# Kernel tuning notes

Hardware: AMD Instinct MI355X
Metric: run time of the kernel (lower is better)

## Reference

```python
import jax, jax.numpy as jnp
import numpy as np

# dims: batch, history P, horizon Q, hidden D, nodes N, cells C=H*W, Z channels
B_, P_, Q_, D_, N_, C_, H_, W_, CZ = 16, 12, 12, 64, 2000, 1024, 32, 32, 2
K_DIFF = 3  # max diffusion step of DCGRUCell -> K+1 Chebyshev terms


def _mlp2(x, w1, b1, w2, b2):
    return jax.nn.relu(x @ w1 + b1) @ w2 + b2


def _st_embedding(SE, TE, sw1, sb1, sw2, sb2, tw1, tb1, tw2, tb2):
    # GMAN-style spatio-temporal embedding: SE (M,D), TE (B,P,2) ints
    se = _mlp2(SE, sw1, sb1, sw2, sb2)                                  # (M, D)
    te = jnp.concatenate([jax.nn.one_hot(TE[..., 0], 7, dtype=SE.dtype),
                          jax.nn.one_hot(TE[..., 1], 288, dtype=SE.dtype)], axis=-1)
    te = _mlp2(te, tw1, tb1, tw2, tb2)                                  # (B, P, D)
    return se[None, None] + te[:, :, None, :]                           # (B, P, M, D)


def _scaled_laplacian(adj):
    # DCRNN 'laplacian' filter: L_tilde = 2 L / lambda_max - I, lambda_max ~= 2
    A = jnp.maximum(adj, adj.T)
    d = A.sum(axis=1)
    dinv = jnp.where(d > 0, jax.lax.rsqrt(d), 0.0)
    eye = jnp.eye(A.shape[0], dtype=A.dtype)
    L = eye - (dinv[:, None] * A) * dinv[None, :]
    return L - eye


def _gconv(x, L, K):
    # Chebyshev diffusion features: x (B,N,F) -> (B,N,F*(K+1))
    xs = [x, jnp.einsum('nm,bmf->bnf', L, x)]
    for _ in range(2, K + 1):
        xs.append(2.0 * jnp.einsum('nm,bmf->bnf', L, xs[-1]) - xs[-2])
    b, n, f = x.shape
    return jnp.stack(xs, axis=-1).reshape(b, n, f * (K + 1))


def _hard_sigmoid(x):
    return jnp.clip(0.2 * x + 0.5, 0.0, 1.0)


def _conv2d(x, w):
    return jax.lax.conv_general_dilated(x, w, (1, 1), 'SAME',
        dimension_numbers=('NHWC', 'HWIO', 'NHWC'))


def _forward(X, Z, TE, adj_gg, adj_gr, gumbel_noise, se_x, se_z, movement_logits,
             stex_se_w1, stex_se_b1, stex_se_w2, stex_se_b2,
             stex_te_w1, stex_te_b1, stex_te_w2, stex_te_b2,
             stez_se_w1, stez_se_b1, stez_se_w2, stez_se_b2,
             stez_te_w1, stez_te_b1, stez_te_w2, stez_te_b2,
             fcs_z_w1, fcs_z_b1, fcs_z_w2, fcs_z_b2,
             fcs_x_in_w1, fcs_x_in_b1, fcs_x_in_w2, fcs_x_in_b2,
             mov_fc_w, mov_fc_b,
             fcs_x_out_w1, fcs_x_out_b1, fcs_x_out_w2, fcs_x_out_b2,
             convlstm_wx, convlstm_wh,
             dcgru_gate_w, dcgru_gate_b, dcgru_cand_w, dcgru_cand_b):
    B = X.shape[0]
    TEp = TE.astype(jnp.int32)[:, :P_, :]
    # --- cell branch ---
    STEZ = _st_embedding(se_z, TEp, stez_se_w1, stez_se_b1, stez_se_w2, stez_se_b2,
                         stez_te_w1, stez_te_b1, stez_te_w2, stez_te_b2)
    Zf = _mlp2(Z, fcs_z_w1, fcs_z_b1, fcs_z_w2, fcs_z_b2) + STEZ          # (B,P,C,D)
    Zg = Zf.reshape(B, P_, H_, W_, D_)
    def clstm_step(carry, x):
        h, c = carry
        gates = _conv2d(x, convlstm_wx) + _conv2d(h, convlstm_wh)         # (B,H,W,4D)
        i, f, g, o = jnp.split(gates, 4, axis=-1)
        c = _hard_sigmoid(f) * c + _hard_sigmoid(i) * jnp.tanh(g)
        h = _hard_sigmoid(o) * jnp.tanh(c)
        return (h, c), h
    hc0 = (jnp.zeros((B, H_, W_, D_), X.dtype), jnp.zeros((B, H_, W_, D_), X.dtype))
    _, hs = jax.lax.scan(clstm_step, hc0, jnp.swapaxes(Zg, 0, 1))
    Zc = jnp.swapaxes(hs, 0, 1).reshape(B, P_, C_, D_)
    # gumbel-softmax routing over cells (soft, tau=1)
    g = -jnp.log(-jnp.log(gumbel_noise + 1e-20) + 1e-20)
    mZ = jax.nn.softmax(movement_logits + g, axis=-1)                     # (C,C)
    Zc = jnp.einsum('cd,bpdk->bpck', mZ, Zc)
    Zc = jax.nn.relu(Zc @ mov_fc_w + mov_fc_b)
    ZX = jnp.einsum('nc,bpck->bpnk', adj_gr, Zc)                          # (B,P,N,D)
    # --- node branch ---
    STEX = _st_embedding(se_x, TEp, stex_se_w1, stex_se_b1, stex_se_w2, stex_se_b2,
                         stex_te_w1, stex_te_b1, stex_te_w2, stex_te_b2)
    Xf = _mlp2(X[..., None], fcs_x_in_w1, fcs_x_in_b1, fcs_x_in_w2, fcs_x_in_b2) + STEX + ZX
    L = _scaled_laplacian(adj_gg)
    def dcgru_step(h, x):
        xh = jnp.concatenate([x, h], axis=-1)                             # (B,N,2D)
        ru = jax.nn.sigmoid(_gconv(xh, L, K_DIFF) @ dcgru_gate_w + dcgru_gate_b)
        r, u = jnp.split(ru, 2, axis=-1)
        cnd = jnp.tanh(_gconv(jnp.concatenate([x, r * h], axis=-1), L, K_DIFF)
                       @ dcgru_cand_w + dcgru_cand_b)
        return u * h + (1.0 - u) * cnd, None
    h_last, _ = jax.lax.scan(dcgru_step, jnp.zeros((B, N_, D_), X.dtype),
                             jnp.swapaxes(Xf, 0, 1))                      # (B,N,D)
    Y = _mlp2(h_last, fcs_x_out_w1, fcs_x_out_b1, fcs_x_out_w2, fcs_x_out_b2)  # (B,N,Q)
    return jnp.transpose(Y, (0, 2, 1))                                    # (B,Q,N)


def setup_inputs() -> dict:
    key = jax.random.key(0)
    ks = iter(jax.random.split(key, 64))
    def rn(shape, s=0.05):
        return jax.random.normal(next(ks), shape, dtype=jnp.float32) * s
    def ru(shape):
        return jax.random.uniform(next(ks), shape, dtype=jnp.float32)
    z = lambda *s: jnp.zeros(s, jnp.float32)
    NM = K_DIFF + 1
    inp = {
        'X': rn((B_, P_, N_), 1.0),
        'Z': rn((B_, P_, C_, CZ), 1.0),
        'TE': jax.random.randint(next(ks), (B_, P_ + Q_, 2), 0, 7, dtype=jnp.int32),
        'adj_gg': ru((N_, N_)),
        'adj_gr': ru((N_, C_)) * 0.01,
        'gumbel_noise': jnp.clip(ru((C_, C_)), 1e-6, 1.0 - 1e-6),
        'se_x': rn((N_, D_)), 'se_z': rn((C_, D_)),
        'movement_logits': rn((C_, C_)),
        'stex_se_w1': rn((D_, D_)), 'stex_se_b1': z(D_), 'stex_se_w2': rn((D_, D_)), 'stex_se_b2': z(D_),
        'stex_te_w1': rn((295, D_)), 'stex_te_b1': z(D_), 'stex_te_w2': rn((D_, D_)), 'stex_te_b2': z(D_),
        'stez_se_w1': rn((D_, D_)), 'stez_se_b1': z(D_), 'stez_se_w2': rn((D_, D_)), 'stez_se_b2': z(D_),
        'stez_te_w1': rn((295, D_)), 'stez_te_b1': z(D_), 'stez_te_w2': rn((D_, D_)), 'stez_te_b2': z(D_),
        'fcs_z_w1': rn((CZ, D_)), 'fcs_z_b1': z(D_), 'fcs_z_w2': rn((D_, D_)), 'fcs_z_b2': z(D_),
        'fcs_x_in_w1': rn((1, D_)), 'fcs_x_in_b1': z(D_), 'fcs_x_in_w2': rn((D_, D_)), 'fcs_x_in_b2': z(D_),
        'mov_fc_w': rn((D_, D_)), 'mov_fc_b': z(D_),
        'fcs_x_out_w1': rn((D_, D_)), 'fcs_x_out_b1': z(D_), 'fcs_x_out_w2': rn((D_, Q_)), 'fcs_x_out_b2': z(Q_),
        'convlstm_wx': rn((3, 3, D_, 4 * D_)), 'convlstm_wh': rn((3, 3, D_, 4 * D_)),
        'dcgru_gate_w': rn((2 * D_ * NM, 2 * D_)), 'dcgru_gate_b': z(2 * D_),
        'dcgru_cand_w': rn((2 * D_ * NM, D_)), 'dcgru_cand_b': z(D_),
    }
    return inp


def reference(X, Z, TE, adj_gg, adj_gr, gumbel_noise, se_x, se_z, movement_logits,
              stex_se_w1, stex_se_b1, stex_se_w2, stex_se_b2,
              stex_te_w1, stex_te_b1, stex_te_w2, stex_te_b2,
              stez_se_w1, stez_se_b1, stez_se_w2, stez_se_b2,
              stez_te_w1, stez_te_b1, stez_te_w2, stez_te_b2,
              fcs_z_w1, fcs_z_b1, fcs_z_w2, fcs_z_b2,
              fcs_x_in_w1, fcs_x_in_b1, fcs_x_in_w2, fcs_x_in_b2,
              mov_fc_w, mov_fc_b,
              fcs_x_out_w1, fcs_x_out_b1, fcs_x_out_w2, fcs_x_out_b2,
              convlstm_wx, convlstm_wh,
              dcgru_gate_w, dcgru_gate_b, dcgru_cand_w, dcgru_cand_b):
    return _forward(X, Z, TE, adj_gg, adj_gr, gumbel_noise, se_x, se_z, movement_logits,
                    stex_se_w1, stex_se_b1, stex_se_w2, stex_se_b2,
                    stex_te_w1, stex_te_b1, stex_te_w2, stex_te_b2,
                    stez_se_w1, stez_se_b1, stez_se_w2, stez_se_b2,
                    stez_te_w1, stez_te_b1, stez_te_w2, stez_te_b2,
                    fcs_z_w1, fcs_z_b1, fcs_z_w2, fcs_z_b2,
                    fcs_x_in_w1, fcs_x_in_b1, fcs_x_in_w2, fcs_x_in_b2,
                    mov_fc_w, mov_fc_b,
                    fcs_x_out_w1, fcs_x_out_b1, fcs_x_out_w2, fcs_x_out_b2,
                    convlstm_wx, convlstm_wh,
                    dcgru_gate_w, dcgru_gate_b, dcgru_cand_w, dcgru_cand_b)
```

## Files before the change

kernel.cpp:

```cpp
#include <hip/hip_runtime.h>
#include <hip/hip_bf16.h>
#include <math.h>

typedef _Float16 fp16;
typedef _Float16 f16x8 __attribute__((ext_vector_type(8)));
typedef float f32x4 __attribute__((ext_vector_type(4)));

#define BB 16
#define PP 12
#define QQ 12
#define NN 2000
#define CC 1024
#define GP 34
#define GP2 1156

static __device__ __forceinline__ float ldf(float v) { return v; }
static __device__ __forceinline__ float ldf(fp16 v) { return (float)v; }
static __device__ __forceinline__ void stf(float* p, float v) { *p = v; }
static __device__ __forceinline__ void stf(fp16* p, float v) { *p = (fp16)v; }

static __device__ __forceinline__ void gload_lds16(const fp16* g, fp16* l) {
  __builtin_amdgcn_global_load_lds(
      (const __attribute__((address_space(1))) void*)g,
      (__attribute__((address_space(3))) void*)l, 16, 0, 0);
// ... 130 lines not shown
}

__global__ void k_add_stez(fp16* __restrict__ dst, const fp16* __restrict__ src,
                           const float* __restrict__ seZ, const float* __restrict__ teZ) {
  long long i = (long long)blockIdx.x * 256 + threadIdx.x;
  if (i >= (long long)BB * PP * CC * 64) return;
  int j = (int)(i & 63);
  long long row = i >> 6;
  int c = (int)(row & 1023);
  int bp = (int)(row >> 10);
  int pc = ((c >> 5) + 1) * GP + (c & 31) + 1;
  dst[((long long)bp * GP2 + pc) * 64 + j] =
      (fp16)((float)src[i] + seZ[c * 64 + j] + teZ[bp * 64 + j]);
}

template <typename TA, typename TB, typename TC>
__global__ __launch_bounds__(256) void gemm_t(
    const TA* __restrict__ A, int lda, long long sA,
    const TB* __restrict__ Bm, int ldb, long long sB,
    TC* Cm, int ldc, long long sC,
    const TC* S, long long sS,
    const float* __restrict__ bias,
    int M, int Ncols, int K, float alpha, float beta, int act) {
  int bz = blockIdx.z;
  A += (long long)bz * sA;
  Bm += (long long)bz * sB;
  Cm += (long long)bz * sC;
  if (S) S += (long long)bz * sS;
  const int row0 = blockIdx.x * 64, col0 = blockIdx.y * 64;
  __shared__ float As[16][68];
  __shared__ float Bs[16][68];
  int tid = threadIdx.x, tx = tid & 15, ty = tid >> 4;
  float acc[4][4] = {};
  for (int k0 = 0; k0 < K; k0 += 16) {
#pragma unroll
    for (int j = 0; j < 4; ++j) {
      int e = tid + 256 * j;
      int m = e >> 4, kk = e & 15;
      int gm = row0 + m;
      As[kk][m] = (gm < M) ? ldf(A[(long long)gm * lda + k0 + kk]) : 0.f;
    }
#pragma unroll
    for (int j = 0; j < 4; ++j) {
      int e = tid + 256 * j;
      int kk = e >> 6, n = e & 63;
      int gn = col0 + n;
      Bs[kk][n] = (gn < Ncols) ? ldf(Bm[(long long)(k0 + kk) * ldb + gn]) : 0.f;
    }
    __syncthreads();
#pragma unroll
    for (int kk = 0; kk < 16; ++kk) {
      float a[4], bb[4];
#pragma unroll
      for (int i = 0; i < 4; ++i) a[i] = As[kk][ty * 4 + i];
#pragma unroll
      for (int j = 0; j < 4; ++j) bb[j] = Bs[kk][tx * 4 + j];
#pragma unroll
      for (int i = 0; i < 4; ++i)
#pragma unroll
        for (int j = 0; j < 4; ++j) acc[i][j] = fmaf(a[i], bb[j], acc[i][j]);
    }
    __syncthreads();
  }
#pragma unroll
  for (int i = 0; i < 4; ++i) {
    int r = row0 + ty * 4 + i;
    if (r >= M) continue;
#pragma unroll
    for (int j = 0; j < 4; ++j) {
      int cn = col0 + tx * 4 + j;
      if (cn >= Ncols) continue;
      float v = alpha * acc[i][j];
      if (bias) v += bias[cn];
      if (S) v += beta * ldf(S[(long long)r * ldc + cn]);
      if (act == 1) v = fmaxf(v, 0.f);
      else if (act == 2) v = 1.f / (1.f + expf(-v));
      else if (act == 3) v = tanhf(v);
      stf(&Cm[(long long)r * ldc + cn], v);
    }
  }
}

template <int MT, int MODE>
__global__ __launch_bounds__(256) void mfma2(
    const fp16* __restrict__ A, int lda,
    const fp16* __restrict__ B, int ldb, long long bBatch, int bShift, long long bSlab,
    int bHi,
    fp16* __restrict__ C, int ldc, long long cBatch,
    const float* __restrict__ bias,
    fp16* __restrict__ rhOut, const fp16* __restrict__ hIn, long long xStride,
    const fp16* __restrict__ uIn, long long uStride,
    const fp16* __restrict__ xB, long long xZ,
    int M, int Ncols, int K, float alpha) {
  __shared__ fp16 As[MT][40];
  __shared__ fp16 Bs[64][40];
  const int z = blockIdx.z;
  const int gm0 = blockIdx.x * MT, n0 = blockIdx.y * 64;
  B += (long long)z * bBatch;
  C += (long long)z * cBatch;
  if (rhOut) rhOut += (long long)z * xStride;
  if (hIn) hIn += (long long)z * xStride;
  if (uIn) uIn += (long long)z * uStride;
  if (xB) xB += (long long)z * xZ;
  const int tid = threadIdx.x;
  const int lane = tid & 63, wv = tid >> 6;
  const int wr = wv >> 1, wc = wv & 1;
  const int quad = lane >> 4, ln = lane & 15;
  const unsigned bMask = (1u << bShift) - 1u;
  constexpr int WM = MT / 32;
  f32x4 acc[WM][2];
#pragma unroll
  for (int i = 0; i < WM; ++i)
#pragma unroll
    for (int j = 0; j < 2; ++j) acc[i][j] = (f32x4){0.f, 0.f, 0.f, 0.f};

  for (int k0 = 0; k0 < K; k0 += 32) {
#pragma unroll
    for (int i = 0; i < MT / 64; ++i) {
      int c = tid + 256 * i;
      int row = c >> 2, seg = c & 3;
      int gm = gm0 + row;
      int kk0 = k0 + seg * 8;
      const fp16* src = A + (long long)gm * lda + kk0;
      if (gm < M && kk0 + 8 <= K) {
        *(f16x8*)&As[row][seg * 8] = *(const f16x8*)src;
      } else {
#pragma unroll
        for (int j = 0; j < 8; ++j)
          As[row][seg * 8 + j] = (gm < M && kk0 + j < K) ? src[j] : (fp16)0.f;
      }
    }
    {
      int kk = k0 + (tid & 31);
      int ngrp = tid >> 5;
      int slab = (int)((unsigned)kk >> bShift);
      int kin = (int)((unsigned)kk & bMask);
      int col = kin + (kin >= 64 ? bHi : 0);
      int n = n0 + ngrp * 8;
      const fp16* src;
      if (xB && slab == 0 && kin < 64)
        src = xB + (long long)kin * 2048 + n;
      else
        src = B + (long long)slab * bSlab + (long long)col * ldb + n;
      if (kk < K && n + 8 <= Ncols) {
        f16x8 v = *(const f16x8*)src;
#pragma unroll
        for (int j = 0; j < 8; ++j) Bs[ngrp * 8 + j][tid & 31] = v[j];
      } else {
#pragma unroll
        for (int j = 0; j < 8; ++j)
          Bs[ngrp * 8 + j][tid & 31] = (kk < K && n + j < Ncols) ? src[j] : (fp16)0.f;
      }
    }
    __syncthreads();
    f16x8 af[WM], bf[2];
#pragma unroll
    for (int wm = 0; wm < WM; ++wm)
      af[wm] = *(const f16x8*)&As[wr * (MT / 2) + wm * 16 + ln][quad * 8];
#pragma unroll
    for (int wn = 0; wn < 2; ++wn)
      bf[wn] = *(const f16x8*)&Bs[wc * 32 + wn * 16 + ln][quad * 8];
#pragma unroll
    for (int wm = 0; wm < WM; ++wm)
#pragma unroll
      for (int wn = 0; wn < 2; ++wn)
        acc[wm][wn] =
            __builtin_amdgcn_mfma_f32_16x16x32_f16(af[wm], bf[wn], acc[wm][wn], 0, 0, 0);
    __syncthreads();
  }
#pragma unroll
  for (int wm = 0; wm < WM; ++wm) {
#pragma unroll
    for (int wn = 0; wn < 2; ++wn) {
#pragma unroll
      for (int r = 0; r < 4; ++r) {
        int gm = gm0 + wr * (MT / 2) + wm * 16 + quad * 4 + r;
        int gn = n0 + wc * 32 + wn * 16 + ln;
        if (gm < M && gn < Ncols) {
          float v = alpha * acc[wm][wn][r];
          v += bias[gm];
          if (MODE == 1) {
            v = 1.f / (1.f + expf(-v));
            C[(long long)gm * ldc + gn] = (fp16)v;
            if (gm < 64) {
              float h = (float)hIn[(long long)gm * 2048 + gn];
              rhOut[(long long)gm * 2048 + gn] = (fp16)(v * h);
            }
          } else {
            v = tanhf(v);
            float u = (float)uIn[(long long)(64 + gm) * NN + gn];
            long long ci = (long long)gm * ldc + gn;
            float h = (float)C[ci];
            C[ci] = (fp16)(u * h + (1.f - u) * v);
          }
        }
      }
    }
  }
}

template <int MT, int NT>
__global__ __launch_bounds__(256) void mfma3(
    const fp16* __restrict__ A, int lda, long long zA, int aMsh, long long aMslab,
    const fp16* __restrict__ B, int ldb, long long zB,
    fp16* __restrict__ C, int ldc, long long zC, int cMsh, long long cMslab, int cNsh,
    long long cNslab,
    const fp16* __restrict__ S, long long zS, float beta,
    const float* __restrict__ rowBias, long long zRB,
    const float* __restrict__ s2T, int s2ld,
    int M, int Ncols, int K, float alpha, int act) {
  __shared__ fp16 As[MT][40];
  __shared__ fp16 Bs[NT][40];
  const int z = blockIdx.z;
  const int gm0 = blockIdx.x * MT, n0 = blockIdx.y * NT;
  A += (long long)z * zA;
  B += (long long)z * zB;
  C += (long long)z * zC;
  if (S) S += (long long)z * zS;
  const int tid = threadIdx.x;
  const int lane = tid & 63, wv = tid >> 6;
  const int wr = wv >> 1, wc = wv & 1;
  const int quad = lane >> 4, ln = lane & 15;
  const unsigned aMmask = (1u << aMsh) - 1u;
  const unsigned cMmask = (1u << cMsh) - 1u;
  const unsigned cNmask = (1u << cNsh) - 1u;
  constexpr int WM = MT / 32, WN = NT / 32;
  f32x4 acc[WM][WN];
#pragma unroll
  for (int i = 0; i < WM; ++i)
#pragma unroll
    for (int j = 0; j < WN; ++j) acc[i][j] = (f32x4){0.f, 0.f, 0.f, 0.f};

  for (int k0 = 0; k0 < K; k0 += 32) {
#pragma unroll
    for (int i = 0; i < MT / 64; ++i) {
      int c = tid + 256 * i;
      int row = c >> 2, seg = c & 3;
      int gm = gm0 + row;
      int kk0 = k0 + seg * 8;
      const fp16* src = A + ((long long)((unsigned)gm >> aMsh)) * aMslab +
                        (long long)(gm & aMmask) * lda + kk0;
      if (gm < M && kk0 + 8 <= K) {
        *(f16x8*)&As[row][seg * 8] = *(const f16x8*)src;
      } else {
#pragma unroll
        for (int j = 0; j < 8; ++j)
          As[row][seg * 8 + j] = (gm < M && kk0 + j < K) ? src[j] : (fp16)0.f;
      }
    }
#pragma unroll
    for (int i = 0; i < NT / 64; ++i) {
      int c = tid + 256 * i;
      int n = c >> 2, seg = c & 3;
      int gn = n0 + n;
      int kk0 = k0 + seg * 8;
      const fp16* src = B + (long long)gn * ldb + kk0;
      if (gn < Ncols && kk0 + 8 <= K) {
        *(f16x8*)&Bs[n][seg * 8] = *(const f16x8*)src;
      } else {
#pragma unroll
        for (int j = 0; j < 8; ++j)
          Bs[n][seg * 8 + j] = (gn < Ncols && kk0 + j < K) ? src[j] : (fp16)0.f;
// ... 68 lines not shown
  const fp16* bSrc[NT / 64];
#pragma unroll
  for (int i = 0; i < MT / 64; ++i) {
    int c = i * 256 + tid;
    int row = c >> 2;
    int lseg = (c & 3) ^ (row & 3);
    int gm = gm0 + row;
    unsigned b = (unsigned)gm >> rsh;
    unsigned wi = (unsigned)gm & ((1u << rsh) - 1u);
    unsigned sel = wi >> ssh;
    unsigned r = wi & ((1u << ssh) - 1u);
    const fp16* ab = sel ? (base1 + (long long)b * z1) : (base0 + (long long)b * z0);
    aSrc[i] = ab + (long long)r * lda + lseg * 8;
  }
#pragma unroll
  for (int i = 0; i < NT / 64; ++i) {
    int c = i * 256 + tid;
    int row = c >> 2;
    int lseg = (c & 3) ^ (row & 3);
    bSrc[i] = B + (long long)(n0 + row) * ldb + lseg * 8;
  }

  f32x4 acc[WM][WN];
#pragma unroll
  for (int i = 0; i < WM; ++i)
#pragma unroll
    for (int j = 0; j < WN; ++j) acc[i][j] = (f32x4){0.f, 0.f, 0.f, 0.f};

  const int sw = (quad ^ (ln & 3)) << 3;

#pragma unroll
  for (int i = 0; i < MT / 64; ++i) gload_lds16(aSrc[i], &As[0][(i * 256 + tid) * 8]);
#pragma unroll
  for (int i = 0; i < NT / 64; ++i) gload_lds16(bSrc[i], &Bs[0][(i * 256 + tid) * 8]);

  const int nk = K >> 5;
  for (int t = 0; t < nk; ++t) {
    const int buf = t & 1;
    __syncthreads();
    if (t + 1 < nk) {
      const int k1 = (t + 1) * 32;
#pragma unroll
      for (int i = 0; i < MT / 64; ++i)
        gload_lds16(aSrc[i] + k1, &As[buf ^ 1][(i * 256 + tid) * 8]);
#pragma unroll
      for (int i = 0; i < NT / 64; ++i)
        gload_lds16(bSrc[i] + k1, &Bs[buf ^ 1][(i * 256 + tid) * 8]);
    }
    f16x8 af[WM], bf[WN];
#pragma unroll
    for (int wm = 0; wm < WM; ++wm) {
      int row = wr * (MT / 2) + wm * 16 + ln;
      af[wm] = *(const f16x8*)&As[buf][row * 32 + sw];
    }
#pragma unroll
    for (int wn = 0; wn < WN; ++wn) {
      int row = wc * (NT / 2) + wn * 16 + ln;
      bf[wn] = *(const f16x8*)&Bs[buf][row * 32 + sw];
    }
#pragma unroll
    for (int wm = 0; wm < WM; ++wm)
#pragma unroll
      for (int wn = 0; wn < WN; ++wn)
        acc[wm][wn] =
            __builtin_amdgcn_mfma_f32_16x16x32_f16(af[wm], bf[wn], acc[wm][wn], 0, 0, 0);
  }
#pragma unroll
  for (int wm = 0; wm < WM; ++wm)
#pragma unroll
    for (int wn = 0; wn < WN; ++wn)
#pragma unroll
      for (int r = 0; r < 4; ++r) {
        int gm = gm0 + wr * (MT / 2) + wm * 16 + quad * 4 + r;
        int gn = n0 + wc * (NT / 2) + wn * 16 + ln;
        long long ci = ((long long)((unsigned)gm >> cMsh)) * cMslab +
                       (long long)(gm & cMmask) * ldc +
                       ((long long)((unsigned)gn >> cNsh)) * cNslab + (gn & cNmask);
        float v = alpha * acc[wm][wn][r];
        if (S) v += beta * (float)S[ci];
        C[ci] = (fp16)v;
      }
}

__global__ __launch_bounds__(256) void k_zxt4(
    const fp16* __restrict__ A1, const fp16* __restrict__ B1,
    const fp16* __restrict__ A2, const fp16* __restrict__ B2,
    fp16* __restrict__ C, const float* __restrict__ teXb, const float* __restrict__ seX) {
  __shared__ fp16 As[2][64 * 32];
  __shared__ fp16 Bs[2][128 * 32];
  const int z = blockIdx.z;
  const int n0 = blockIdx.y * 128;
  A1 += (long long)z * 64 * 1024;
  B2 += (long long)z * 2048 * 64;
  C += (long long)z * 64 * 2048;
  teXb += z * 64;
  const int tid = threadIdx.x;
  const int lane = tid & 63, wv = tid >> 6;
  const int wr = wv >> 1, wc = wv & 1;
  const int quad = lane >> 4, ln = lane & 15;

  const fp16 *a1p, *a2p;
  {
    int row = tid >> 2;
    int lseg = (tid & 3) ^ (row & 3);
    a1p = A1 + (long long)row * 1024 + lseg * 8;
    a2p = A2 + (long long)row * 64 + lseg * 8;
  }
  const fp16 *b1p[2], *b2p[2];
#pragma unroll
  for (int i = 0; i < 2; ++i) {
    int c = tid + 256 * i;
    int row = c >> 2;
    int lseg = (c & 3) ^ (row & 3);
    b1p[i] = B1 + (long long)(n0 + row) * 1024 + lseg * 8;
    b2p[i] = B2 + (long long)(n0 + row) * 64 + lseg * 8;
  }
  f32x4 acc[2][4];
#pragma unroll
  for (int i = 0; i < 2; ++i)
#pragma unroll
    for (int j = 0; j < 4; ++j) acc[i][j] = (f32x4){0.f, 0.f, 0.f, 0.f};

  auto stage = [&](int t, int buf) {
    if (t < 32) {
      int k1 = t * 32;
      gload_lds16(a1p + k1, &As[buf][tid * 8]);
#pragma unroll
      for (int i = 0; i < 2; ++i)
        gload_lds16(b1p[i] + k1, &Bs[buf][(i * 256 + tid) * 8]);
    } else {
      int k1 = (t - 32) * 32;
      gload_lds16(a2p + k1, &As[buf][tid * 8]);
#pragma unroll
      for (int i = 0; i < 2; ++i)
        gload_lds16(b2p[i] + k1, &Bs[buf][(i * 256 + tid) * 8]);
    }
  };
  stage(0, 0);
  const int sw = (quad ^ (ln & 3)) << 3;
  for (int t = 0; t < 34; ++t) {
    const int buf = t & 1;
    __syncthreads();
    if (t + 1 < 34) stage(t + 1, buf ^ 1);
    f16x8 af[2], bf[4];
#pragma unroll
    for (int wm = 0; wm < 2; ++wm) {
      int row = wr * 32 + wm * 16 + ln;
      af[wm] = *(const f16x8*)&As[buf][row * 32 + sw];
    }
#pragma unroll
    for (int wn = 0; wn < 4; ++wn) {
      int row = wc * 64 + wn * 16 + ln;
      bf[wn] = *(const f16x8*)&Bs[buf][row * 32 + sw];
    }
#pragma unroll
    for (int wm = 0; wm < 2; ++wm)
#pragma unroll
      for (int wn = 0; wn < 4; ++wn)
        acc[wm][wn] =
            __builtin_amdgcn_mfma_f32_16x16x32_f16(af[wm], bf[wn], acc[wm][wn], 0, 0, 0);
  }
#pragma unroll
  for (int wm = 0; wm < 2; ++wm)
#pragma unroll
    for (int wn = 0; wn < 4; ++wn)
#pragma unroll
      for (int r = 0; r < 4; ++r) {
        int gm = wr * 32 + wm * 16 + quad * 4 + r;
        int gn = n0 + wc * 64 + wn * 16 + ln;
        float v = (gn < NN) ? (acc[wm][wn][r] + teXb[gm] + seX[(long long)gn * 64 + gm])
                            : 0.f;
        C[(long long)gm * 2048 + gn] = (fp16)v;
      }
}

__global__ __launch_bounds__(256) void k_conv4(
    const fp16* __restrict__ Zfp, const fp16* __restrict__ hp,
    const fp16* __restrict__ wcatT, fp16* __restrict__ gates, int p) {
  __shared__ fp16 As[2][128 * 32];
  __shared__ fp16 Bs[2][64 * 32];
  const int gm0 = blockIdx.x * 128, n0 = blockIdx.y * 64;
  const int tid = threadIdx.x;
  const int lane = tid & 63, wv = tid >> 6;
  const int wr = wv >> 1, wc = wv & 1;
  const int quad = lane >> 4, ln = lane & 15;

  long long aZ[2], aH[2];
#pragma unroll
  for (int i = 0; i < 2; ++i) {
    int c = tid + 256 * i;
    int row = c >> 2;
    int lseg = (c & 3) ^ (row & 3);
    int m = gm0 + row;
    int b = m >> 10, y = (m >> 5) & 31, x = m & 31;
    int pc = (y + 1) * GP + (x + 1);
    aZ[i] = ((long long)(b * PP + p) * GP2 + pc) * 64 + lseg * 8;
    aH[i] = ((long long)b * GP2 + pc) * 64 + lseg * 8;
  }
  const fp16* bBase;
  {
    int row = tid >> 2;
    int lseg = (tid & 3) ^ (row & 3);
    bBase = wcatT + (long long)(n0 + row) * 1152 + lseg * 8;
  }
  f32x4 acc[4][2];
#pragma unroll
  for (int i = 0; i < 4; ++i)
#pragma unroll
    for (int j = 0; j < 2; ++j) acc[i][j] = (f32x4){0.f, 0.f, 0.f, 0.f};

  auto stage = [&](int t, int buf) {
    int tap = (t >> 1) % 9, half = t & 1;
    int srcsel = t >= 18;
    int off = ((tap / 3 - 1) * GP + (tap % 3 - 1)) * 64 + half * 32;
#pragma unroll
    for (int i = 0; i < 2; ++i) {
      const fp16* src = srcsel ? (hp + aH[i] + off) : (Zfp + aZ[i] + off);
      gload_lds16(src, &As[buf][(i * 256 + tid) * 8]);
    }
    gload_lds16(bBase + t * 32, &Bs[buf][tid * 8]);
  };
  stage(0, 0);
  const int sw = (quad ^ (ln & 3)) << 3;
  for (int t = 0; t < 36; ++t) {
    const int buf = t & 1;
    __syncthreads();
    if (t + 1 < 36) stage(t + 1, buf ^ 1);
    f16x8 af[4], bf[2];
#pragma unroll
    for (int wm = 0; wm < 4; ++wm) {
      int row = wr * 64 + wm * 16 + ln;
      af[wm] = *(const f16x8*)&As[buf][row * 32 + sw];
    }
#pragma unroll
    for (int wn = 0; wn < 2; ++wn) {
      int row = wc * 32 + wn * 16 + ln;
      bf[wn] = *(const f16x8*)&Bs[buf][row * 32 + sw];
    }
#pragma unroll
    for (int wm = 0; wm < 4; ++wm)
#pragma unroll
      for (int wn = 0; wn < 2; ++wn)
        acc[wm][wn] =
            __builtin_amdgcn_mfma_f32_16x16x32_f16(af[wm], bf[wn], acc[wm][wn], 0, 0, 0);
  }
#pragma unroll
  for (int wm = 0; wm < 4; ++wm)
#pragma unroll
    for (int wn = 0; wn < 2; ++wn)
#pragma unroll
      for (int r = 0; r < 4; ++r) {
        int gm = gm0 + wr * 64 + wm * 16 + quad * 4 + r;
        int gn = n0 + wc * 32 + wn * 16 + ln;
        gates[(long long)gm * 256 + gn] = (fp16)acc[wm][wn][r];
      }
// ... 23 lines not shown

__global__ void k_tmat(const float* __restrict__ X, const float* __restrict__ w1,
                       const float* __restrict__ b1, fp16* __restrict__ T, long long nrows) {
  long long i = (long long)blockIdx.x * 256 + threadIdx.x;
  if (i >= nrows * 64) return;
  int j = (int)(i & 63);
  long long row = i >> 6;
  int z = (int)(row / NN);
  int n = (int)(row - (long long)z * NN);
  T[(((long long)z * 2048) + n) * 64 + j] = (fp16)fmaxf(X[row] * w1[j] + b1[j], 0.f);
}

__global__ void k_trT(const fp16* __restrict__ U0, float* __restrict__ htmp) {
  long long i = (long long)blockIdx.x * 256 + threadIdx.x;
  if (i >= (long long)BB * NN * 64) return;
  int d = (int)(i & 63);
  long long bn = i >> 6;
  int b = (int)(bn / NN);
  int n = (int)(bn % NN);
  htmp[i] = (float)U0[((long long)b * 192 + 64 + d) * 2048 + n];
}

__global__ void k_out(const float* __restrict__ Y, float* __restrict__ out) {
  int i = blockIdx.x * 256 + threadIdx.x;
  if (i >= BB * QQ * NN) return;
  int n = i % NN;
  int bq = i / NN;
  int b = bq / QQ, q = bq % QQ;
  out[i] = Y[((long long)b * NN + n) * 12 + q];
}

template <typename TA, typename TB, typename TC>
static void launch_gemm(hipStream_t stream, const TA* A, int lda, long long sA,
                        const TB* Bm, int ldb, long long sB, TC* Cm, int ldc, long long sC,
                        const TC* S, long long sS, const float* bias, int M, int Nc, int K,
                        float alpha, float beta, int act, int batch) {
  dim3 g((M + 63) / 64, (Nc + 63) / 64, batch);
  gemm_t<TA, TB, TC><<<g, dim3(256), 0, stream>>>(A, lda, sA, Bm, ldb, sB, Cm, ldc, sC, S,
                                                  sS, bias, M, Nc, K, alpha, beta, act);
}

extern "C" void kernel_launch(void* const* d_in, const int* in_sizes, int n_in,
                              void* d_out, int out_size, void* d_ws, size_t ws_size,
                              hipStream_t stream) {
  char* base = (char*)d_ws;
  size_t off = 0;
  auto alloc_bytes = [&](size_t nb) -> char* {
    char* p = base + off;
    off += (nb + 255) & ~(size_t)255;
    return p;
  };
  auto allocf = [&](size_t n) -> float* { return (float*)alloc_bytes(n * 4); };
  auto alloch = [&](size_t n) -> fp16* { return (fp16*)alloc_bytes(n * 2); };

  const float* X = (const float*)d_in[0];
  const float* Z = (const float*)d_in[1];
  const int* TE = (const int*)d_in[2];
  const float* adj_gg = (const float*)d_in[3];
  const float* adj_gr = (const float*)d_in[4];
  const float* gumbel = (const float*)d_in[5];
  const float* se_x = (const float*)d_in[6];
  const float* se_z = (const float*)d_in[7];
  const float* movement = (const float*)d_in[8];
  auto W = [&](int i) { return (const float*)d_in[i]; };

  fp16* wcatT = alloch((size_t)256 * 1152);
  fp16* gwT = alloch(128 * 512);
  fp16* cwT = alloch(64 * 512);
  fp16* w2T = alloch(64 * 64);
  fp16* w2mT = alloch(64 * 64);
  float* dinv = allocf(NN);
  fp16* LMall = alloch((size_t)6144 * 2048);
  fp16* mZh = alloch((size_t)CC * CC);
  fp16* agh2 = alloch((size_t)2048 * CC);
  float* seZ = allocf(CC * 64);
  float* teZ = allocf(BB * PP * 64);
  float* seX = allocf(NN * 64);
  float* teXb = allocf(BB * PP * 64);
  float* mtmp = allocf(NN * 64);
  float* tetmp = allocf(BB * PP * 64);
  fp16* ruT = alloch((size_t)BB * 128 * NN);
  char* pool = alloc_bytes(50331648);
  fp16* Uall = (fp16*)pool;
  fp16* Zftmp = (fp16*)pool;
  fp16* gates = (fp16*)pool;
  fp16* chh = (fp16*)(pool + 8388608);
  float* ccc = (float*)(pool + 12582912);
  fp16* Zmix = (fp16*)pool;
  fp16* ZmovT = (fp16*)(pool + 25165824);
  fp16* zpool = alloch((size_t)BB * PP * 64 * 2048);
  fp16* Zfp = zpool;
  fp16* ZXt = zpool;
  fp16* Zc = alloch((size_t)BB * PP * CC * 64);

  if (off > ws_size) return;

  const long long uB = 192LL * 2048;
  const long long USL = 16LL * uB;
  const long long ZXB = 12LL * 64 * 2048;
  fp16* Lh = LMall;
  fp16* M2h = LMall + 2048LL * 2048;
  fp16* M3h = LMall + 4096LL * 2048;
  const int KCH = 2016;

  k_wcatT<<<dim3(1152), dim3(256), 0, stream>>>(wcatT, W(39), W(40));
  k_gru_repackT<<<dim3(256), dim3(256), 0, stream>>>(gwT, W(41), 128);
  k_gru_repackT<<<dim3(128), dim3(256), 0, stream>>>(cwT, W(43), 64);
  k_w2T<<<dim3(16), dim3(256), 0, stream>>>(w2T, W(31));
  k_w2T<<<dim3(16), dim3(256), 0, stream>>>(w2mT, W(33));
  k_dinv<<<dim3(NN), dim3(256), 0, stream>>>(adj_gg, dinv);
  hipMemsetAsync(LMall, 0, (size_t)6144 * 2048 * 2, stream);
  k_L<<<dim3((NN * NN + 255) / 256), dim3(256), 0, stream>>>(adj_gg, dinv, Lh);
  mfma4<64, 128><<<dim3(32, 16, 1), dim3(256), 0, stream>>>(
      Lh, Lh, 31, 31, 0LL, 0LL, 2048, Lh, 2048, 0LL, M2h, 2048, 0LL, 31, 0LL, 31, 0LL,
      (const fp16*)nullptr, 2.f, 0.f, KCH);
  k_subdiag<<<dim3((NN + 255) / 256), dim3(256), 0, stream>>>(M2h);
  mfma4<64, 128><<<dim3(32, 16, 1), dim3(256), 0, stream>>>(
      Lh, Lh, 31, 31, 0LL, 0LL, 2048, M2h, 2048, 0LL, M3h, 2048, 0LL, 31, 0LL, 31, 0LL,
      (const fp16*)Lh, 2.f, -1.f, KCH);
  k_gumbel_softmax<<<dim3(CC), dim3(256), 0, stream>>>(movement, gumbel, mZh);
  k_f2h<<<dim3((NN * CC + 255) / 256), dim3(256), 0, stream>>>(agh2, adj_gr,
                                                               (long long)NN * CC);
  hipMemsetAsync(agh2 + (size_t)NN * CC, 0, (size_t)(2048 - NN) * CC * 2, stream);

  launch_gemm(stream, se_z, 64, 0LL, W(17), 64, 0LL, mtmp, 64, 0LL, (float*)nullptr, 0LL,
              W(18), CC, 64, 64, 1.f, 0.f, 1, 1);
  launch_gemm(stream, (const float*)mtmp, 64, 0LL, W(19), 64, 0LL, seZ, 64, 0LL,
              (float*)nullptr, 0LL, W(20), CC, 64, 64, 1.f, 0.f, 0, 1);
  k_te<<<dim3((BB * PP * 64 + 255) / 256), dim3(256), 0, stream>>>(TE, W(21), W(22), tetmp);
  launch_gemm(stream, (const float*)tetmp, 64, 0LL, W(23), 64, 0LL, teZ, 64, 0LL,
              (float*)nullptr, 0LL, W(24), BB * PP, 64, 64, 1.f, 0.f, 0, 1);
  launch_gemm(stream, se_x, 64, 0LL, W(9), 64, 0LL, mtmp, 64, 0LL, (float*)nullptr, 0LL,
              W(10), NN, 64, 64, 1.f, 0.f, 1, 1);
  launch_gemm(stream, (const float*)mtmp, 64, 0LL, W(11), 64, 0LL, seX, 64, 0LL,
              (float*)nullptr, 0LL, W(12), NN, 64, 64, 1.f, 0.f, 0, 1);
  k_te<<<dim3((BB * PP * 64 + 255) / 256), dim3(256), 0, stream>>>(TE, W(13), W(14), tetmp);
  launch_gemm(stream, (const float*)tetmp, 64, 0LL, W(15), 64, 0LL, teXb, 64, 0LL,
              (float*)nullptr, 0LL, W(16), BB * PP, 64, 64, 1.f, 0.f, 0, 1);
  k_addb<<<dim3((BB * PP * 64 + 255) / 256), dim3(256), 0, stream>>>(teXb, W(32),
                                                                     BB * PP * 64);

  long long nZ = (long long)BB * PP * CC * 64;
  k_zf1<<<dim3((int)((nZ + 255) / 256)), dim3(256), 0, stream>>>(Z, W(25), W(26), Zc);
  launch_gemm(stream, (const fp16*)Zc, 64, 0LL, W(27), 64, 0LL, Zftmp, 64, 0LL,
              (fp16*)nullptr, 0LL, W(28), BB * PP * CC, 64, 64, 1.f, 0.f, 0, 1);
  hipMemsetAsync(zpool, 0, (size_t)BB * PP * GP2 * 64 * 2, stream);
  k_add_stez<<<dim3((int)((nZ + 255) / 256)), dim3(256), 0, stream>>>(Zfp, Zftmp, seZ, teZ);

  hipMemsetAsync(chh, 0, (size_t)BB * GP2 * 64 * 2, stream);
  hipMemsetAsync(ccc, 0, (size_t)BB * CC * 64 * 4, stream);
  for (int p = 0; p < PP; ++p) {
    k_conv4<<<dim3(BB * CC / 128, 4), dim3(256), 0, stream>>>(Zfp, chh, wcatT, gates, p);
    k_clstm_update<<<dim3((int)(((long long)BB * CC * 64 + 255) / 256)), dim3(256), 0,
                     stream>>>(gates, ccc, chh, Zc, p);
  }

  mfma4<128, 64><<<dim3(8, 1, 192), dim3(256), 0, stream>>>(
      mZh, mZh, 31, 31, 0LL, 0LL, CC, (const fp16*)Zc, CC, (long long)64 * CC, Zmix, 64,
      (long long)CC * 64, 31, 0LL, 31, 0LL, (const fp16*)nullptr, 1.f, 0.f, CC);
  mfma3<64, 128><<<dim3(1, 8, 192), dim3(256), 0, stream>>>(
      w2mT, 64, 0LL, 31, 0LL, Zmix, 64, (long long)CC * 64, ZmovT, CC, (long long)64 * CC,
      31, 0LL, 31, 0LL, (const fp16*)nullptr, 0LL, 0.f, W(34), 0LL, nullptr, 0, 64, CC, 64,
      1.f, 1);

  fp16* Tmat = Zc;
  for (int half = 0; half < 2; ++half) {
    long long z0 = 96LL * half;
    k_tmat<<<dim3((int)((96LL * NN * 64 + 255) / 256)), dim3(256), 0, stream>>>(
        X + z0 * NN, W(29), W(30), Tmat, 96LL * NN);
    k_zxt4<<<dim3(1, 16, 96), dim3(256), 0, stream>>>(
        ZmovT + z0 * 64 * CC, agh2, w2T, Tmat, ZXt + z0 * 64 * 2048, teXb + z0 * 64, seX);
  }

  fp16* U0 = Uall;
  fp16* U1 = Uall + USL;
  hipMemsetAsync(U0, 0, (size_t)USL * 2, stream);
  for (int p = 0; p < PP; ++p) {
    const fp16* xP = ZXt + (long long)p * 64 * 2048;
    mfma4<128, 128><<<dim3(16, 48, 1), dim3(256), 0, stream>>>(
        xP, U0 + 64 * 2048, 7, 6, ZXB, uB, 2048, LMall, 2048, 0LL, U1, 2048, 0LL, 7, uB,
        11, USL, (const fp16*)nullptr, 1.f, 0.f, KCH);
    mfma2<128, 1><<<dim3(1, 32, BB), dim3(256), 0, stream>>>(
        gwT, 512, Uall, 2048, uB, 7, USL, 0, ruT, NN, (long long)128 * NN, W(42),
        U0 + 128 * 2048, U0 + 64 * 2048, uB, (const fp16*)nullptr, 0LL, xP, ZXB, 128, NN,
        512, 1.f);
    mfma4<64, 128><<<dim3(16, 48, 1), dim3(256), 0, stream>>>(
        U0 + 128 * 2048, U0, 6, 31, uB, 0LL, 2048, LMall, 2048, 0LL, U1 + 128 * 2048, 2048,
        0LL, 6, uB, 11, USL, (const fp16*)nullptr, 1.f, 0.f, KCH);
    mfma2<64, 2><<<dim3(1, 32, BB), dim3(256), 0, stream>>>(
        cwT, 512, Uall, 2048, uB, 7, USL, 64, U0 + 64 * 2048, 2048, uB, W(44),
        (fp16*)nullptr, (const fp16*)nullptr, 0LL, (const fp16*)ruT, (long long)128 * NN,
        xP, ZXB, 64, NN, 512, 1.f);
  }

  float* htmp = (float*)Zc;
  float* out1 = (float*)(Zc + 5120000);
  float* out2 = (float*)(Zc + 10240000);
  k_trT<<<dim3((int)(((long long)BB * NN * 64 + 255) / 256)), dim3(256), 0, stream>>>(U0,
                                                                                      htmp);
  launch_gemm(stream, (const float*)htmp, 64, 0LL, W(35), 64, 0LL, out1, 64, 0LL,
              (float*)nullptr, 0LL, W(36), BB * NN, 64, 64, 1.f, 0.f, 1, 1);
  launch_gemm(stream, (const float*)out1, 64, 0LL, W(37), 12, 0LL, out2, 12, 0LL,
              (float*)nullptr, 0LL, W(38), BB * NN, 12, 64, 1.f, 0.f, 0, 1);
  k_out<<<dim3((BB * QQ * NN + 255) / 256), dim3(256), 0, stream>>>(out2, (float*)d_out);
}
```

Measured before the change: 3.220 ms.

## Transpose diffusion GEMM outputs to node-major layout and split ZX transform

The per-step Chebyshev diffusion GEMMs move to a new double-buffered kernel (mfma6) that puts the Laplacian in the A operand. It writes node-major outputs (Tn, Tn2), which the gate and candidate GEMMs (mfma5) then read with contiguous vector loads, replacing the strided per-element transposed B loads. The fused two-phase ZX kernel is split into a large batched GEMM over all 192 slices plus a small finishing kernel that adds the Tmat projection, the embeddings and the existing result. Boundary checks in the A and B loads are dropped, which assumes the dimensions are exact multiples of the tiles. Extra buffer space (3 slabs) is used inside the pool.

```diff
diff --git a/kernel.cpp b/kernel.cpp
--- a/kernel.cpp
+++ b/kernel.cpp
@@ -236,31 +236,31 @@
 }
 
 template <int MT, int MODE>
-__global__ __launch_bounds__(256) void mfma2(
+__global__ __launch_bounds__(256) void mfma5(
     const fp16* __restrict__ A, int lda,
-    const fp16* __restrict__ B, int ldb, long long bBatch, int bShift, long long bSlab,
-    int bHi,
+    const fp16* __restrict__ U0base, long long uZ, int bHi,
+    const fp16* __restrict__ xB, long long xZ,
+    const fp16* __restrict__ Tn, long long TnSlab,
+    const fp16* __restrict__ Tn2, long long Tn2Slab,
     fp16* __restrict__ C, int ldc, long long cBatch,
     const float* __restrict__ bias,
-    fp16* __restrict__ rhOut, const fp16* __restrict__ hIn, long long xStride,
+    fp16* __restrict__ rhOut, const fp16* __restrict__ hIn,
     const fp16* __restrict__ uIn, long long uStride,
-    const fp16* __restrict__ xB, long long xZ,
-    int M, int Ncols, int K, float alpha) {
+    int M, int Ncols, int K) {
   __shared__ fp16 As[MT][40];
   __shared__ fp16 Bs[64][40];
   const int z = blockIdx.z;
   const int gm0 = blockIdx.x * MT, n0 = blockIdx.y * 64;
-  B += (long long)z * bBatch;
+  const fp16* U0z = U0base + (long long)z * uZ;
+  const fp16* xBz = xB + (long long)z * xZ;
   C += (long long)z * cBatch;
-  if (rhOut) rhOut += (long long)z * xStride;
-  if (hIn) hIn += (long long)z * xStride;
+  if (rhOut) rhOut += (long long)z * uZ;
+  if (hIn) hIn += (long long)z * uZ;
   if (uIn) uIn += (long long)z * uStride;
-  if (xB) xB += (long long)z * xZ;
   const int tid = threadIdx.x;
   const int lane = tid & 63, wv = tid >> 6;
   const int wr = wv >> 1, wc = wv & 1;
   const int quad = lane >> 4, ln = lane & 15;
-  const unsigned bMask = (1u << bShift) - 1u;
   constexpr int WM = MT / 32;
   f32x4 acc[WM][2];
 #pragma unroll
@@ -273,37 +273,30 @@
     for (int i = 0; i < MT / 64; ++i) {
       int c = tid + 256 * i;
       int row = c >> 2, seg = c & 3;
-      int gm = gm0 + row;
-      int kk0 = k0 + seg * 8;
-      const fp16* src = A + (long long)gm * lda + kk0;
-      if (gm < M && kk0 + 8 <= K) {
-        *(f16x8*)&As[row][seg * 8] = *(const f16x8*)src;
-      } else {
-#pragma unroll
-        for (int j = 0; j < 8; ++j)
-          As[row][seg * 8 + j] = (gm < M && kk0 + j < K) ? src[j] : (fp16)0.f;
-      }
+      *(f16x8*)&As[row][seg * 8] =
+          *(const f16x8*)(A + (long long)(gm0 + row) * lda + k0 + seg * 8);
     }
     {
-      int kk = k0 + (tid & 31);
-      int ngrp = tid >> 5;
-      int slab = (int)((unsigned)kk >> bShift);
-      int kin = (int)((unsigned)kk & bMask);
-      int col = kin + (kin >= 64 ? bHi : 0);
-      int n = n0 + ngrp * 8;
-      const fp16* src;
-      if (xB && slab == 0 && kin < 64)
-        src = xB + (long long)kin * 2048 + n;
-      else
-        src = B + (long long)slab * bSlab + (long long)col * ldb + n;
-      if (kk < K && n + 8 <= Ncols) {
+      int slab = k0 >> 7;
+      if (slab == 0) {
+        int kin = k0 + (tid & 31);
+        int ngrp = tid >> 5;
+        int n = n0 + ngrp * 8;
+        const fp16* src = (kin < 64) ? (xBz + (long long)kin * 2048 + n)
+                                     : (U0z + (long long)(kin + bHi) * 2048 + n);
         f16x8 v = *(const f16x8*)src;
 #pragma unroll
         for (int j = 0; j < 8; ++j) Bs[ngrp * 8 + j][tid & 31] = v[j];
       } else {
-#pragma unroll
-        for (int j = 0; j < 8; ++j)
-          Bs[ngrp * 8 + j][tid & 31] = (kk < K && n + j < Ncols) ? src[j] : (fp16)0.f;
+        int n = tid >> 2, seg = tid & 3;
+        int kin0 = (k0 & 127) + seg * 8;
+        long long node = n0 + n;
+        const fp16* src;
+        if (MODE == 1 || kin0 < 64)
+          src = Tn + (long long)(slab - 1) * TnSlab + node * 2048 + z * 128 + kin0;
+        else
+          src = Tn2 + (long long)(slab - 1) * Tn2Slab + node * 1024 + z * 64 + (kin0 - 64);
+        *(f16x8*)&Bs[n][seg * 8] = *(const f16x8*)src;
       }
     }
     __syncthreads();
@@ -331,7 +324,7 @@
         int gm = gm0 + wr * (MT / 2) + wm * 16 + quad * 4 + r;
         int gn = n0 + wc * 32 + wn * 16 + ln;
         if (gm < M && gn < Ncols) {
-          float v = alpha * acc[wm][wn][r];
+          float v = acc[wm][wn][r];
           v += bias[gm];
           if (MODE == 1) {
             v = 1.f / (1.f + expf(-v));
@@ -566,77 +559,146 @@
       }
 }
 
-__global__ __launch_bounds__(256) void k_zxt4(
-    const fp16* __restrict__ A1, const fp16* __restrict__ B1,
-    const fp16* __restrict__ A2, const fp16* __restrict__ B2,
-    fp16* __restrict__ C, const float* __restrict__ teXb, const float* __restrict__ seX) {
-  __shared__ fp16 As[2][64 * 32];
-  __shared__ fp16 Bs[2][128 * 32];
+template <int MT, int NT>
+__global__ __launch_bounds__(256) void mfma6(
+    const fp16* __restrict__ A, int lda,
+    const fp16* __restrict__ b0, const fp16* __restrict__ b1, int rsh, int ssh,
+    long long z0, long long z1, int ldb,
+    fp16* __restrict__ C, int ldc, int cMsh, long long cMslab,
+    int K) {
+  __shared__ fp16 As[2][MT * 32];
+  __shared__ fp16 Bs[2][NT * 32];
+  const int tid = threadIdx.x;
+  const int gm0 = blockIdx.x * MT, n0 = blockIdx.y * NT;
+  const unsigned cMmask = (1u << cMsh) - 1u;
+  const int lane = tid & 63, wv = tid >> 6;
+  const int wr = wv >> 1, wc = wv & 1;
+  const int quad = lane >> 4, ln = lane & 15;
+  constexpr int WM = MT / 32, WN = NT / 32;
+
+  const fp16* aSrc[MT / 64];
+  const fp16* bSrc[NT / 64];
+#pragma unroll
+  for (int i = 0; i < MT / 64; ++i) {
+    int c = i * 256 + tid;
+    int row = c >> 2;
+    int lseg = (c & 3) ^ (row & 3);
+    aSrc[i] = A + (long long)(gm0 + row) * lda + lseg * 8;
+  }
+#pragma unroll
+  for (int i = 0; i < NT / 64; ++i) {
+    int c = i * 256 + tid;
+    int row = c >> 2;
+    int lseg = (c & 3) ^ (row & 3);
+    int gn = n0 + row;
+    unsigned b = (unsigned)gn >> rsh;
+    unsigned wi = (unsigned)gn & ((1u << rsh) - 1u);
+    unsigned sel = wi >> ssh;
+    unsigned r = wi & ((1u << ssh) - 1u);
+    const fp16* bb = sel ? (b1 + (long long)b * z1) : (b0 + (long long)b * z0);
+    bSrc[i] = bb + (long long)r * ldb + lseg * 8;
+  }
+
+  f32x4 acc[WM][WN];
+#pragma unroll
+  for (int i = 0; i < WM; ++i)
+#pragma unroll
+    for (int j = 0; j < WN; ++j) acc[i][j] = (f32x4){0.f, 0.f, 0.f, 0.f};
+
+  const int sw = (quad ^ (ln & 3)) << 3;
+
+#pragma unroll
+  for (int i = 0; i < MT / 64; ++i) gload_lds16(aSrc[i], &As[0][(i * 256 + tid) * 8]);
+#pragma unroll
+  for (int i = 0; i < NT / 64; ++i) gload_lds16(bSrc[i], &Bs[0][(i * 256 + tid) * 8]);
+
+  const int nk = K >> 5;
+  for (int t = 0; t < nk; ++t) {
+    const int buf = t & 1;
+    __syncthreads();
+    if (t + 1 < nk) {
+      const int k1 = (t + 1) * 32;
+#pragma unroll
+      for (int i = 0; i < MT / 64; ++i)
+        gload_lds16(aSrc[i] + k1, &As[buf ^ 1][(i * 256 + tid) * 8]);
+#pragma unroll
+      for (int i = 0; i < NT / 64; ++i)
+        gload_lds16(bSrc[i] + k1, &Bs[buf ^ 1][(i * 256 + tid) * 8]);
+    }
+    f16x8 af[WM], bf[WN];
+#pragma unroll
+    for (int wm = 0; wm < WM; ++wm) {
+      int row = wr * (MT / 2) + wm * 16 + ln;
+      af[wm] = *(const f16x8*)&As[buf][row * 32 + sw];
+    }
+#pragma unroll
+    for (int wn = 0; wn < WN; ++wn) {
+      int row = wc * (NT / 2) + wn * 16 + ln;
+      bf[wn] = *(const f16x8*)&Bs[buf][row * 32 + sw];
+    }
+#pragma unroll
+    for (int wm = 0; wm < WM; ++wm)
+#pragma unroll
+      for (int wn = 0; wn < WN; ++wn)
+        acc[wm][wn] =
+            __builtin_amdgcn_mfma_f32_16x16x32_f16(af[wm], bf[wn], acc[wm][wn], 0, 0, 0);
+  }
+#pragma unroll
+  for (int wm = 0; wm < WM; ++wm)
+#pragma unroll
+    for (int wn = 0; wn < WN; ++wn)
+#pragma unroll
+      for (int r = 0; r < 4; ++r) {
+        int gm = gm0 + wr * (MT / 2) + wm * 16 + quad * 4 + r;
+        int gn = n0 + wc * (NT / 2) + wn * 16 + ln;
+        long long ci = ((long long)((unsigned)gm >> cMsh)) * cMslab +
+                       (long long)(gm & cMmask) * ldc + gn;
+        C[ci] = (fp16)acc[wm][wn][r];
+      }
+}
+
+__global__ __launch_bounds__(256) void k_zxtfin(
+    const fp16* __restrict__ w2T, const fp16* __restrict__ Tmat,
+    fp16* __restrict__ ZXt, const float* __restrict__ teXb, const float* __restrict__ seX) {
+  __shared__ fp16 As[64][72];
+  __shared__ fp16 Bs[128][72];
   const int z = blockIdx.z;
   const int n0 = blockIdx.y * 128;
-  A1 += (long long)z * 64 * 1024;
-  B2 += (long long)z * 2048 * 64;
-  C += (long long)z * 64 * 2048;
-  teXb += z * 64;
+  const fp16* Tz = Tmat + (long long)z * 2048 * 64;
+  fp16* Cz = ZXt + (long long)z * 64 * 2048;
+  const float* tb = teXb + z * 64;
   const int tid = threadIdx.x;
   const int lane = tid & 63, wv = tid >> 6;
   const int wr = wv >> 1, wc = wv & 1;
   const int quad = lane >> 4, ln = lane & 15;
-
-  const fp16 *a1p, *a2p;
-  {
-    int row = tid >> 2;
-    int lseg = (tid & 3) ^ (row & 3);
-    a1p = A1 + (long long)row * 1024 + lseg * 8;
-    a2p = A2 + (long long)row * 64 + lseg * 8;
-  }
-  const fp16 *b1p[2], *b2p[2];
 #pragma unroll
   for (int i = 0; i < 2; ++i) {
     int c = tid + 256 * i;
-    int row = c >> 2;
-    int lseg = (c & 3) ^ (row & 3);
-    b1p[i] = B1 + (long long)(n0 + row) * 1024 + lseg * 8;
-    b2p[i] = B2 + (long long)(n0 + row) * 64 + lseg * 8;
-  }
+    int row = c >> 3, seg = c & 7;
+    *(f16x8*)&As[row][seg * 8] = *(const f16x8*)(w2T + row * 64 + seg * 8);
+  }
+#pragma unroll
+  for (int i = 0; i < 4; ++i) {
+    int c = tid + 256 * i;
+    int row = c >> 3, seg = c & 7;
+    *(f16x8*)&Bs[row][seg * 8] =
+        *(const f16x8*)(Tz + (long long)(n0 + row) * 64 + seg * 8);
+  }
+  __syncthreads();
   f32x4 acc[2][4];
 #pragma unroll
   for (int i = 0; i < 2; ++i)
 #pragma unroll
     for (int j = 0; j < 4; ++j) acc[i][j] = (f32x4){0.f, 0.f, 0.f, 0.f};
-
-  auto stage = [&](int t, int buf) {
-    if (t < 32) {
-      int k1 = t * 32;
-      gload_lds16(a1p + k1, &As[buf][tid * 8]);
-#pragma unroll
-      for (int i = 0; i < 2; ++i)
-        gload_lds16(b1p[i] + k1, &Bs[buf][(i * 256 + tid) * 8]);
-    } else {
-      int k1 = (t - 32) * 32;
-      gload_lds16(a2p + k1, &As[buf][tid * 8]);
-#pragma unroll
-      for (int i = 0; i < 2; ++i)
-        gload_lds16(b2p[i] + k1, &Bs[buf][(i * 256 + tid) * 8]);
-    }
-  };
-  stage(0, 0);
-  const int sw = (quad ^ (ln & 3)) << 3;
-  for (int t = 0; t < 34; ++t) {
-    const int buf = t & 1;
-    __syncthreads();
-    if (t + 1 < 34) stage(t + 1, buf ^ 1);
+#pragma unroll
+  for (int kt = 0; kt < 2; ++kt) {
     f16x8 af[2], bf[4];
 #pragma unroll
-    for (int wm = 0; wm < 2; ++wm) {
-      int row = wr * 32 + wm * 16 + ln;
-      af[wm] = *(const f16x8*)&As[buf][row * 32 + sw];
-    }
-#pragma unroll
-    for (int wn = 0; wn < 4; ++wn) {
-      int row = wc * 64 + wn * 16 + ln;
-      bf[wn] = *(const f16x8*)&Bs[buf][row * 32 + sw];
-    }
+    for (int wm = 0; wm < 2; ++wm)
+      af[wm] = *(const f16x8*)&As[wr * 32 + wm * 16 + ln][kt * 32 + quad * 8];
+#pragma unroll
+    for (int wn = 0; wn < 4; ++wn)
+      bf[wn] = *(const f16x8*)&Bs[wc * 64 + wn * 16 + ln][kt * 32 + quad * 8];
 #pragma unroll
     for (int wm = 0; wm < 2; ++wm)
 #pragma unroll
@@ -652,9 +714,11 @@
       for (int r = 0; r < 4; ++r) {
         int gm = wr * 32 + wm * 16 + quad * 4 + r;
         int gn = n0 + wc * 64 + wn * 16 + ln;
-        float v = (gn < NN) ? (acc[wm][wn][r] + teXb[gm] + seX[(long long)gn * 64 + gm])
-                            : 0.f;
-        C[(long long)gm * 2048 + gn] = (fp16)v;
+        long long ci = (long long)gm * 2048 + gn;
+        float v = 0.f;
+        if (gn < NN)
+          v = acc[wm][wn][r] + (float)Cz[ci] + tb[gm] + seX[(long long)gn * 64 + gm];
+        Cz[ci] = (fp16)v;
       }
 }
 
@@ -844,7 +908,6 @@
   fp16* ruT = alloch((size_t)BB * 128 * NN);
   char* pool = alloc_bytes(50331648);
   fp16* Uall = (fp16*)pool;
-  fp16* Zftmp = (fp16*)pool;
   fp16* gates = (fp16*)pool;
   fp16* chh = (fp16*)(pool + 8388608);
   float* ccc = (float*)(pool + 12582912);
@@ -904,10 +967,11 @@
 
   long long nZ = (long long)BB * PP * CC * 64;
   k_zf1<<<dim3((int)((nZ + 255) / 256)), dim3(256), 0, stream>>>(Z, W(25), W(26), Zc);
-  launch_gemm(stream, (const fp16*)Zc, 64, 0LL, W(27), 64, 0LL, Zftmp, 64, 0LL,
+  launch_gemm(stream, (const fp16*)Zc, 64, 0LL, W(27), 64, 0LL, (fp16*)pool, 64, 0LL,
               (fp16*)nullptr, 0LL, W(28), BB * PP * CC, 64, 64, 1.f, 0.f, 0, 1);
   hipMemsetAsync(zpool, 0, (size_t)BB * PP * GP2 * 64 * 2, stream);
-  k_add_stez<<<dim3((int)((nZ + 255) / 256)), dim3(256), 0, stream>>>(Zfp, Zftmp, seZ, teZ);
+  k_add_stez<<<dim3((int)((nZ + 255) / 256)), dim3(256), 0, stream>>>(Zfp, (fp16*)pool,
+                                                                      seZ, teZ);
 
   hipMemsetAsync(chh, 0, (size_t)BB * GP2 * 64 * 2, stream);
   hipMemsetAsync(ccc, 0, (size_t)BB * CC * 64 * 4, stream);
@@ -925,34 +989,40 @@
       31, 0LL, 31, 0LL, (const fp16*)nullptr, 0LL, 0.f, W(34), 0LL, nullptr, 0, 64, CC, 64,
       1.f, 1);
 
+  mfma4<128, 128><<<dim3(96, 16, 1), dim3(256), 0, stream>>>(
+      ZmovT, ZmovT, 31, 31, 0LL, 0LL, 1024, agh2, 1024, 0LL, ZXt, 2048, 0LL, 31, 0LL, 31,
+      0LL, (const fp16*)nullptr, 1.f, 0.f, 1024);
+
   fp16* Tmat = Zc;
   for (int half = 0; half < 2; ++half) {
     long long z0 = 96LL * half;
     k_tmat<<<dim3((int)((96LL * NN * 64 + 255) / 256)), dim3(256), 0, stream>>>(
         X + z0 * NN, W(29), W(30), Tmat, 96LL * NN);
-    k_zxt4<<<dim3(1, 16, 96), dim3(256), 0, stream>>>(
-        ZmovT + z0 * 64 * CC, agh2, w2T, Tmat, ZXt + z0 * 64 * 2048, teXb + z0 * 64, seX);
+    k_zxtfin<<<dim3(1, 16, 96), dim3(256), 0, stream>>>(
+        w2T, Tmat, ZXt + z0 * 64 * 2048, teXb + z0 * 64, seX);
   }
 
   fp16* U0 = Uall;
-  fp16* U1 = Uall + USL;
+  fp16* Tn = Uall + USL;
+  fp16* Tn2 = Uall + 3 * USL;
+  const long long TnSlab = 2048LL * 2048;
+  const long long Tn2Slab = 2048LL * 1024;
   hipMemsetAsync(U0, 0, (size_t)USL * 2, stream);
   for (int p = 0; p < PP; ++p) {
     const fp16* xP = ZXt + (long long)p * 64 * 2048;
-    mfma4<128, 128><<<dim3(16, 48, 1), dim3(256), 0, stream>>>(
-        xP, U0 + 64 * 2048, 7, 6, ZXB, uB, 2048, LMall, 2048, 0LL, U1, 2048, 0LL, 7, uB,
-        11, USL, (const fp16*)nullptr, 1.f, 0.f, KCH);
-    mfma2<128, 1><<<dim3(1, 32, BB), dim3(256), 0, stream>>>(
-        gwT, 512, Uall, 2048, uB, 7, USL, 0, ruT, NN, (long long)128 * NN, W(42),
-        U0 + 128 * 2048, U0 + 64 * 2048, uB, (const fp16*)nullptr, 0LL, xP, ZXB, 128, NN,
-        512, 1.f);
-    mfma4<64, 128><<<dim3(16, 48, 1), dim3(256), 0, stream>>>(
-        U0 + 128 * 2048, U0, 6, 31, uB, 0LL, 2048, LMall, 2048, 0LL, U1 + 128 * 2048, 2048,
-        0LL, 6, uB, 11, USL, (const fp16*)nullptr, 1.f, 0.f, KCH);
-    mfma2<64, 2><<<dim3(1, 32, BB), dim3(256), 0, stream>>>(
-        cwT, 512, Uall, 2048, uB, 7, USL, 64, U0 + 64 * 2048, 2048, uB, W(44),
-        (fp16*)nullptr, (const fp16*)nullptr, 0LL, (const fp16*)ruT, (long long)128 * NN,
-        xP, ZXB, 64, NN, 512, 1.f);
+    mfma6<128, 128><<<dim3(48, 16), dim3(256), 0, stream>>>(
+        LMall, 2048, xP, U0 + 64 * 2048, 7, 6, ZXB, uB, 2048, Tn, 2048, 11, TnSlab, KCH);
+    mfma5<128, 1><<<dim3(1, 32, BB), dim3(256), 0, stream>>>(
+        gwT, 512, U0, uB, 0, xP, ZXB, Tn, TnSlab, (const fp16*)nullptr, 0LL, ruT, NN,
+        (long long)128 * NN, W(42), U0 + 128 * 2048, U0 + 64 * 2048,
+        (const fp16*)nullptr, 0LL, 128, NN, 512);
+    mfma6<128, 128><<<dim3(48, 8), dim3(256), 0, stream>>>(
+        LMall, 2048, U0 + 128 * 2048, U0 + 128 * 2048, 6, 6, uB, uB, 2048, Tn2, 1024, 11,
+        Tn2Slab, KCH);
+    mfma5<64, 2><<<dim3(1, 32, BB), dim3(256), 0, stream>>>(
+        cwT, 512, U0, uB, 64, xP, ZXB, Tn, TnSlab, Tn2, Tn2Slab, U0 + 64 * 2048, 2048, uB,
+        W(44), (fp16*)nullptr, (const fp16*)nullptr, (const fp16*)ruT, (long long)128 * NN,
+        64, NN, 512);
   }
 
   float* htmp = (float*)Zc;
```

Result: faster. 3.118 ms (-3.2%).
